# Kernel optimization log

Hardware: AMD Instinct MI355X
Metric: run time of the kernel (lower is better)

The kernel has to match this reference:

```python
import jax, jax.numpy as jnp
import numpy as np

D = 128; H = 8; DH = D // H; L = 3
NA = 8000; NL = 32000; N = NA + NL
E1 = 65536; D_RPE = 5; D_FFN = 2 * D; RF_H = 128


def _ln(x, eps=1e-5):
    mu = x.mean(-1, keepdims=True)
    var = ((x - mu) ** 2).mean(-1, keepdims=True)
    return (x - mu) * jax.lax.rsqrt(var + eps)


def _rms(x, eps=1e-8):
    rms = jnp.sqrt((x ** 2).sum(-1, keepdims=True)) / np.sqrt(x.shape[-1]).astype(np.float32)
    return x / (rms + eps)


def _seg_softmax(logits, idx, n):
    m = jax.ops.segment_max(logits, idx, num_segments=n)
    e = jnp.exp(logits - m[idx])
    s = jax.ops.segment_sum(e, idx, num_segments=n)
    return e / (s[idx] + 1e-16)


def _gat_layer(x, edge_attr, src, dst, mp_W, mp_b, eu_W, eu_b, Wq, Wk, Wv, Wo, fW1, fb1, fW2, fb2):
    E = src.shape[0]
    # build_mem: gather endpoints, project, LN, ReLU
    cat = jnp.concatenate([x[dst], x[src], edge_attr], axis=-1)       # [E, 3D]
    mem = jax.nn.relu(_ln(cat @ mp_W.T + mp_b))                       # [E, D]
    delta = jax.nn.relu(_ln(mem @ eu_W.T + eu_b))                     # edge_update_block
    edge_attr = _ln(edge_attr + delta)                                # edge_norm
    # multi-head edge attention: q from receiver node, k/v from mem
    q = (x[dst] @ Wq.T).reshape(E, H, DH)
    k = (mem @ Wk.T).reshape(E, H, DH)
    v = (mem @ Wv.T).reshape(E, H, DH)
    logits = (q * k).sum(-1) / np.sqrt(DH).astype(np.float32)         # [E, H]
    attn = _seg_softmax(logits, dst, N)                               # segment softmax over receivers
    msg = (attn[..., None] * v).reshape(E, D) @ Wo.T                  # [E, D]
    aggr = jax.ops.segment_sum(msg, dst, num_segments=N)              # scatter-add
    x = _ln(x + aggr)
    h = jax.nn.relu(x @ fW1.T + fb1) @ fW2.T + fb2
    x = _ln(x + h)
    return x, edge_attr


def _ddc(x_cur, prev_list, W1, b1, W2, b2):
    xs = jnp.stack(prev_list, axis=1)                                 # [N, k, D]
    a = jax.nn.gelu(_rms(x_cur) @ W1.T + b1, approximate=False)
    a = jax.nn.softmax(a @ W2.T + b2, axis=-1)                        # [N, k]
    return (a[..., None] * xs).sum(1)


def setup_inputs() -> dict:
    key = jax.random.key(0)
    ks = iter(jax.random.split(key, 48))
    def nrm(shape, fan_in):
        return jax.random.normal(next(ks), shape, jnp.float32) * np.float32(1.0 / np.sqrt(fan_in))
    inp = {}
    inp['actors'] = jax.random.normal(next(ks), (NA, D), jnp.float32)
    inp['lanes'] = jax.random.normal(next(ks), (NL, D), jnp.float32)
    inp['a2a_attr'] = jax.random.normal(next(ks), (E1, D), jnp.float32)
    inp['l2l_attr'] = jax.random.normal(next(ks), (E1, D), jnp.float32)
    inp['a2l_rpe'] = jax.random.normal(next(ks), (E1, D_RPE), jnp.float32)
    inp['rpe_W'] = nrm((D, D_RPE), D_RPE); inp['rpe_b'] = jnp.zeros((D,), jnp.float32)
    inp['mp_W'] = nrm((L, D, 3 * D), 3 * D); inp['mp_b'] = jnp.zeros((L, D), jnp.float32)
    inp['eu_W'] = nrm((L, D, D), D); inp['eu_b'] = jnp.zeros((L, D), jnp.float32)
    inp['Wq'] = nrm((L, D, D), D); inp['Wk'] = nrm((L, D, D), D)
    inp['Wv'] = nrm((L, D, D), D); inp['Wo'] = nrm((L, D, D), D)
    inp['ffn_W1'] = nrm((L, D_FFN, D), D); inp['ffn_b1'] = jnp.zeros((L, D_FFN), jnp.float32)
    inp['ffn_W2'] = nrm((L, D, D_FFN), D_FFN); inp['ffn_b2'] = jnp.zeros((L, D), jnp.float32)
    inp['rf0_W1'] = nrm((RF_H, D), D); inp['rf0_b1'] = jnp.zeros((RF_H,), jnp.float32)
    inp['rf0_W2'] = nrm((1, RF_H), RF_H); inp['rf0_b2'] = jnp.zeros((1,), jnp.float32)
    inp['rf1_W1'] = nrm((RF_H, D), D); inp['rf1_b1'] = jnp.zeros((RF_H,), jnp.float32)
    inp['rf1_W2'] = nrm((2, RF_H), RF_H); inp['rf1_b2'] = jnp.zeros((2,), jnp.float32)
    inp['a2a_edges'] = jax.random.randint(next(ks), (2, E1), 0, N, jnp.int32)
    inp['l2l_edges'] = jax.random.randint(next(ks), (2, E1), 0, N, jnp.int32)
    inp['a2l_edges'] = jax.random.randint(next(ks), (2, E1), 0, N, jnp.int32)
    return inp


def reference(actors, lanes, a2a_attr, l2l_attr, a2l_rpe, rpe_W, rpe_b,
              mp_W, mp_b, eu_W, eu_b, Wq, Wk, Wv, Wo,
              ffn_W1, ffn_b1, ffn_W2, ffn_b2,
              rf0_W1, rf0_b1, rf0_W2, rf0_b2,
              rf1_W1, rf1_b1, rf1_W2, rf1_b2,
              a2a_edges, l2l_edges, a2l_edges):
    token = jnp.concatenate([actors, lanes], axis=0)                  # single scene: actors then lanes
    edge_index = jnp.concatenate([a2a_edges, l2l_edges, a2l_edges], axis=1)
    a2l_attr = jax.nn.relu(_ln(a2l_rpe @ rpe_W.T + rpe_b))            # proj_a2l_l2a_rpe
    edge_attr = jnp.concatenate([a2a_attr, l2l_attr, a2l_attr], axis=0)
    src, dst = edge_index[0], edge_index[1]
    rf = [(rf0_W1, rf0_b1, rf0_W2, rf0_b2), (rf1_W1, rf1_b1, rf1_W2, rf1_b2)]
    token_list = [token]
    for i in range(L):
        token, edge_attr = _gat_layer(token, edge_attr, src, dst,
                                      mp_W[i], mp_b[i], eu_W[i], eu_b[i],
                                      Wq[i], Wk[i], Wv[i], Wo[i],
                                      ffn_W1[i], ffn_b1[i], ffn_W2[i], ffn_b2[i])
        if i < L - 1:
            token = _ddc(token, token_list, *rf[i])
        token_list.append(token)
    return token[:NA], token[NA:]
```

## Files before the change

kernel.cpp:

```cpp
#include <hip/hip_runtime.h>
#include <hip/hip_bf16.h>

using bf16 = __hip_bfloat16;
typedef __bf16 bf16x8 __attribute__((ext_vector_type(8)));
typedef float f32x4 __attribute__((ext_vector_type(4)));

constexpr int DD   = 128;
constexpr int NACT = 8000;
constexpr int NN   = 40000;
constexpr int E1   = 65536;
constexpr int EE   = 3 * E1;

#define BM 128

__device__ __forceinline__ void gload16(const void* g, void* l) {
  __builtin_amdgcn_global_load_lds((const __attribute__((address_space(1))) void*)g,
                                   (__attribute__((address_space(3))) void*)l, 16, 0, 0);
}

__device__ __forceinline__ int edge_dst(int e, const int* e0, const int* e1, const int* e2) {
  int ty = e >> 16, idx = e & 65535;
  const int* ep = (ty == 0) ? e0 : ((ty == 1) ? e1 : e2);
  return ep[E1 + idx];
}
__device__ __forceinline__ int edge_src(int e, const int* e0, const int* e1, const int* e2) {
  int ty = e >> 16, idx = e & 65535;
  const int* ep = (ty == 0) ? e0 : ((ty == 1) ? e1 : e2);
  return ep[idx];
}

__device__ __forceinline__ void mfma_step(const bf16* A0, int lda, const bf16* B0, int ldb,
                                          f32x4 acc[4][4], int wm, int wn, int lane) {
  const int lr = lane & 15;
  const int lk = (lane >> 4) * 8;
  bf16x8 a[4], b[4];
#pragma unroll
  for (int i = 0; i < 4; i++)
    a[i] = *(const bf16x8*)(A0 + (size_t)(wm * 64 + i * 16 + lr) * lda + lk);
#pragma unroll
  for (int j = 0; j < 4; j++)
    b[j] = *(const bf16x8*)(B0 + (size_t)(wn * 64 + j * 16 + lr) * ldb + lk);
#pragma unroll
  for (int i = 0; i < 4; i++)
#pragma unroll
    for (int j = 0; j < 4; j++)
      acc[i][j] = __builtin_amdgcn_mfma_f32_16x16x32_bf16(a[i], b[j], acc[i][j], 0, 0, 0);
}

__device__ __forceinline__ void mfma_swz(const bf16* A0, const bf16* B0,
                                         f32x4 acc[4][4], int wm, int wn, int lane) {
  const int lr = lane & 15;
  const int g  = lane >> 4;
  const int sw = (g ^ ((lr >> 1) & 3)) * 8;
  bf16x8 a[4], b[4];
#pragma unroll
  for (int i = 0; i < 4; i++)
    a[i] = *(const bf16x8*)(A0 + (wm * 64 + i * 16 + lr) * 32 + sw);
#pragma unroll
  for (int j = 0; j < 4; j++)
    b[j] = *(const bf16x8*)(B0 + (wn * 64 + j * 16 + lr) * 32 + sw);
#pragma unroll
  for (int i = 0; i < 4; i++)
#pragma unroll
    for (int j = 0; j < 4; j++)
      acc[i][j] = __builtin_amdgcn_mfma_f32_16x16x32_bf16(a[i], b[j], acc[i][j], 0, 0, 0);
}

__device__ __forceinline__ void mfma_mixed(const bf16* Am, int lda, const bf16* B0,
                                           f32x4 acc[4][4], int wm, int wn, int lane) {
  const int lr = lane & 15;
  const int g  = lane >> 4;
  const int sw = (g ^ ((lr >> 1) & 3)) * 8;
  bf16x8 a[4], b[4];
#pragma unroll
  for (int i = 0; i < 4; i++)
    a[i] = *(const bf16x8*)(Am + (size_t)(wm * 64 + i * 16 + lr) * lda + g * 8);
#pragma unroll
  for (int j = 0; j < 4; j++)
    b[j] = *(const bf16x8*)(B0 + (wn * 64 + j * 16 + lr) * 32 + sw);
#pragma unroll
  for (int i = 0; i < 4; i++)
#pragma unroll
    for (int j = 0; j < 4; j++)
      acc[i][j] = __builtin_amdgcn_mfma_f32_16x16x32_bf16(a[i], b[j], acc[i][j], 0, 0, 0);
}

__device__ __forceinline__ void row_ln_stats(const f32x4 acc[4][4], float* red_s,
                                             float* red_q, int wm, int wn, int lane) {
  const int lr = lane & 15, lg = lane >> 4;
#pragma unroll
  for (int i = 0; i < 4; i++) {
#pragma unroll
    for (int q = 0; q < 4; q++) {
      float s = acc[i][0][q] + acc[i][1][q] + acc[i][2][q] + acc[i][3][q];
      float t = acc[i][0][q] * acc[i][0][q] + acc[i][1][q] * acc[i][1][q]
              + acc[i][2][q] * acc[i][2][q] + acc[i][3][q] * acc[i][3][q];
#pragma unroll
      for (int off = 1; off < 16; off <<= 1) {
        s += __shfl_xor(s, off);
        t += __shfl_xor(t, off);
      }
      if (lr == 0) {
        int row = wm * 64 + i * 16 + lg * 4 + q;
        red_s[wn * 128 + row] = s;
        red_q[wn * 128 + row] = t;
      }
    }
  }
}

template<int LAST>
__global__ __launch_bounds__(256, 3) void k_fused(
    const bf16* __restrict__ Wmp, const bf16* __restrict__ W2,
    const float* __restrict__ mpb, const float* __restrict__ eub,
    bf16* eah, const bf16* __restrict__ x0h,
    const bf16* __restrict__ qh, bf16* vout,
    float* __restrict__ logi, unsigned* __restrict__ nmax,
    const int* __restrict__ e0, const int* __restrict__ e1, const int* __restrict__ e2)
{
  __shared__ __align__(16) char smem[46080];
  bf16* const mem_s = (bf16*)smem;
  bf16* const Bs2   = (bf16*)(smem + 34816);
  float* const red_s = (float*)(smem + 43008);
  float* const red_q = (float*)(smem + 44032);
  int* const sdst = (int*)(smem + 45056);
  int* const ssrc = (int*)(smem + 45568);

  const int tid = threadIdx.x;
  const int bm0 = blockIdx.x * BM;
  const int lane = tid & 63, w = tid >> 6, wm = w >> 1, wn = w & 1;
  const int swzE = ((lane & 3) ^ ((lane >> 3) & 3)) * 8;

  if (tid < 128) sdst[tid] = edge_dst(bm0 + tid, e0, e1, e2);
  else           ssrc[tid - 128] = edge_src(bm0 + tid - 128, e0, e1, e2);
  __syncthreads();
  const int mr0 = w * 16 + (lane >> 2), mr1 = 64 + w * 16 + (lane >> 2);
  const int rd0 = sdst[mr0], rd1 = sdst[mr1];
  const int rs0 = ssrc[mr0], rs1 = ssrc[mr1];
  const bf16* pd0 = x0h + (size_t)rd0 * DD + swzE;
  const bf16* pd1 = x0h + (size_t)rd1 * DD + swzE;
  const bf16* ps0 = x0h + (size_t)rs0 * DD + swzE;
  const bf16* ps1 = x0h + (size_t)rs1 * DD + swzE;
  const bf16* pe0 = eah + (size_t)(bm0 + mr0) * DD + swzE;
  const bf16* pe1 = eah + (size_t)(bm0 + mr1) * DD + swzE;
  const bf16* pB0 = Wmp + (size_t)mr0 * 384 + swzE;
  const bf16* pB1 = Wmp + (size_t)mr1 * 384 + swzE;
  const bf16* pW20 = W2 + (size_t)mr0 * DD + swzE;
  const bf16* pW21 = W2 + (size_t)mr1 * DD + swzE;

  auto STAGE1 = [&](int kb, int buf) {
    const bf16 *a0, *a1;
    const int k4 = (kb & 3) * 32;
    if (kb < 4)      { a0 = pd0 + k4; a1 = pd1 + k4; }
    else if (kb < 8) { a0 = ps0 + k4; a1 = ps1 + k4; }
    else             { a0 = pe0 + k4; a1 = pe1 + k4; }
    char* base = smem + buf * 16384;
    gload16(a0, base + w * 1024);
    gload16(a1, base + 4096 + w * 1024);
    gload16(pB0 + kb * 32, base + 8192 + w * 1024);
    gload16(pB1 + kb * 32, base + 12288 + w * 1024);
  };

  f32x4 acc[4][4] = {};
  STAGE1(0, 0);
  __syncthreads();
  int buf = 0;
#pragma unroll
  for (int kb = 0; kb < 12; kb++) {
    if (kb < 11) STAGE1(kb + 1, buf ^ 1);
    mfma_swz((const bf16*)(smem + buf * 16384), (const bf16*)(smem + buf * 16384 + 8192),
             acc, wm, wn, lane);
    __syncthreads();
    buf ^= 1;
  }

  const int lr = lane & 15, lg = lane >> 4;
  const int colb = wn * 64 + lr;
  const int rowb = wm * 64 + lg * 4;

#pragma unroll
  for (int j = 0; j < 4; j++) {
    float bj = mpb[colb + j * 16];
#pragma unroll
    for (int i = 0; i < 4; i++)
#pragma unroll
      for (int q = 0; q < 4; q++) acc[i][j][q] += bj;
  }
  row_ln_stats(acc, red_s, red_q, wm, wn, lane);
  __syncthreads();
#pragma unroll
  for (int i = 0; i < 4; i++) {
#pragma unroll
    for (int q = 0; q < 4; q++) {
      int row = rowb + i * 16 + q;
      float Sm = red_s[row] + red_s[128 + row];
      float Qs = red_q[row] + red_q[128 + row];
      float mu = Sm * 0.0078125f;
      float var = Qs * 0.0078125f - mu * mu;
      float inv = 1.0f / sqrtf(var + 1e-5f);
#pragma unroll
      for (int j = 0; j < 4; j++)
        mem_s[row * 136 + colb + j * 16] =
            __float2bfloat16(fmaxf((acc[i][j][q] - mu) * inv, 0.f));
    }
  }

  auto GEMM2 = [&](int voff, f32x4 a2[4][4]) {
#pragma unroll 1
    for (int kb = 0; kb < 4; kb++) {
      __syncthreads();
      gload16(pW20 + voff + kb * 32, smem + 34816 + w * 1024);
      gload16(pW21 + voff + kb * 32, smem + 34816 + 4096 + w * 1024);
      __syncthreads();
      mfma_mixed(mem_s + kb * 32, 136, Bs2, a2, wm, wn, lane);
    }
  };
  auto store_tile = [&](bf16* dst) {
#pragma unroll
    for (int c = 0; c < 8; c++) {
      int off = c * 2048 + tid * 8;
      int row = off >> 7, col = off & 127;
      *(uint4*)(dst + (size_t)bm0 * DD + off) = *(uint4*)&mem_s[row * 136 + col];
    }
  };

  if constexpr (LAST == 0) {
    f32x4 acc2[4][4] = {};
    GEMM2(0, acc2);
#pragma unroll
    for (int j = 0; j < 4; j++) {
      float bj = eub[colb + j * 16];
#pragma unroll
      for (int i = 0; i < 4; i++)
#pragma unroll
        for (int q = 0; q < 4; q++) acc2[i][j][q] += bj;
    }
    __syncthreads();
    row_ln_stats(acc2, red_s, red_q, wm, wn, lane);
    __syncthreads();
#pragma unroll
    for (int i = 0; i < 4; i++) {
#pragma unroll
      for (int q = 0; q < 4; q++) {
        int row = rowb + i * 16 + q;
        float Sm = red_s[row] + red_s[128 + row];
        float Qs = red_q[row] + red_q[128 + row];
        float mu = Sm * 0.0078125f;
        float var = Qs * 0.0078125f - mu * mu;
        float inv = 1.0f / sqrtf(var + 1e-5f);
        int r = bm0 + row;
#pragma unroll
        for (int j = 0; j < 4; j++) {
          float d = fmaxf((acc2[i][j][q] - mu) * inv, 0.f);
          float eo = __bfloat162float(eah[(size_t)r * DD + colb + j * 16]);
          acc2[i][j][q] = eo + d;
        }
      }
    }
    __syncthreads();
    row_ln_stats(acc2, red_s, red_q, wm, wn, lane);
    __syncthreads();
#pragma unroll
    for (int i = 0; i < 4; i++) {
#pragma unroll
      for (int q = 0; q < 4; q++) {
        int row = rowb + i * 16 + q;
        float Sm = red_s[row] + red_s[128 + row];
        float Qs = red_q[row] + red_q[128 + row];
        float mu = Sm * 0.0078125f;
        float var = Qs * 0.0078125f - mu * mu;
        float inv = 1.0f / sqrtf(var + 1e-5f);
#pragma unroll
        for (int j = 0; j < 4; j++)
          mem_s[row * 136 + colb + j * 16] =
              __float2bfloat16((acc2[i][j][q] - mu) * inv);
      }
    }
    __syncthreads();
    store_tile(eah);
  } else {
    f32x4 acc2[4][4] = {};
    GEMM2(0, acc2);
#pragma unroll
    for (int i = 0; i < 4; i++) {
#pragma unroll
      for (int q = 0; q < 4; q++) {
        int row = rowb + i * 16 + q;
        int dst = sdst[row];
#pragma unroll
        for (int j = 0; j < 4; j++) {
          int h = wn * 4 + j;
          float qv = __bfloat162float(qh[(size_t)dst * DD + h * 16 + lr]);
          float p = acc2[i][j][q] * qv;
#pragma unroll
          for (int off = 1; off < 16; off <<= 1) p += __shfl_xor(p, off);
          if (lr == 0) {
            p *= 0.25f;
            int e = bm0 + row;
            logi[(size_t)e * 8 + h] = p;
            unsigned u = __float_as_uint(p);
            u = (u & 0x80000000u) ? ~u : (u | 0x80000000u);
            atomicMax(nmax + (size_t)dst * 8 + h, u);
          }
        }
      }
    }
    f32x4 acc3[4][4] = {};
    GEMM2(128 * DD, acc3);
    __syncthreads();
#pragma unroll
    for (int i = 0; i < 4; i++)
#pragma unroll
      for (int q = 0; q < 4; q++) {
        int row = rowb + i * 16 + q;
#pragma unroll
        for (int j = 0; j < 4; j++)
          mem_s[row * 136 + colb + j * 16] = __float2bfloat16(acc3[i][j][q]);
      }
    __syncthreads();
    store_tile(vout);
  }
}

template<int EPI>
__global__ __launch_bounds__(256, 3) void k_gemmG(
    const bf16* __restrict__ A, const bf16* __restrict__ B, void* __restrict__ out,
    const float* __restrict__ bias, const float* __restrict__ aux,
    int M, int K, int lda, int ldc)
{
  __shared__ __align__(16) char smem[36864];
  bf16* const stg = (bf16*)smem;
  float* const red_s = (float*)(smem + 34816);
  float* const red_q = (float*)(smem + 35840);

  const int tid = threadIdx.x, lane = tid & 63, w = tid >> 6;
  const int wm = w >> 1, wn = w & 1;
  const int bm0 = blockIdx.x * BM, bn0 = blockIdx.y * BM;
  const int swzE = ((lane & 3) ^ ((lane >> 3) & 3)) * 8;

  const bf16* pA[2];
  const bf16* pB[2];
#pragma unroll
  for (int r = 0; r < 2; r++) {
    int ra = bm0 + r * 64 + w * 16 + (lane >> 2);
    if (ra > M - 1) ra = M - 1;
    pA[r] = A + (size_t)ra * lda + swzE;
    pB[r] = B + (size_t)(bn0 + r * 64 + w * 16 + (lane >> 2)) * K + swzE;
  }
  auto STAGE = [&](int kb, int buf) {
#pragma unroll
    for (int r = 0; r < 2; r++) {
      gload16(pA[r] + kb * 32, smem + buf * 8192 + r * 4096 + w * 1024);
      gload16(pB[r] + kb * 32, smem + 16384 + buf * 8192 + r * 4096 + w * 1024);
    }
  };

  f32x4 acc[4][4] = {};
  const int KB = K >> 5;
  STAGE(0, 0);
  __syncthreads();
  int buf = 0;
#pragma unroll 1
  for (int kb = 0; kb < KB; kb++) {
    if (kb + 1 < KB) STAGE(kb + 1, buf ^ 1);
    mfma_swz((const bf16*)(smem + buf * 8192), (const bf16*)(smem + 16384 + buf * 8192),
             acc, wm, wn, lane);
    __syncthreads();
    buf ^= 1;
  }

  const int lr = lane & 15, lg = lane >> 4;
  const int colb = wn * 64 + lr;
  const int rowb = wm * 64 + lg * 4;

  if constexpr (EPI == 1 || EPI == 5) {
    if constexpr (EPI == 5) {
#pragma unroll
      for (int j = 0; j < 4; j++) {
        float b = bias[bn0 + colb + j * 16];
#pragma unroll
        for (int i = 0; i < 4; i++)
#pragma unroll
          for (int q = 0; q < 4; q++) acc[i][j][q] = fmaxf(acc[i][j][q] + b, 0.f);
      }
    }
#pragma unroll
    for (int i = 0; i < 4; i++)
#pragma unroll
      for (int q = 0; q < 4; q++) {
        int row = rowb + i * 16 + q;
#pragma unroll
        for (int j = 0; j < 4; j++)
          stg[row * 136 + colb + j * 16] = __float2bfloat16(acc[i][j][q]);
      }
    __syncthreads();
#pragma unroll
    for (int c = 0; c < 8; c++) {
      int off = c * 2048 + tid * 8;
      int row = off >> 7, col = off & 127;
      int r = bm0 + row;
      if (r < M)
        *(uint4*)((bf16*)out + (size_t)r * ldc + bn0 + col) = *(uint4*)&stg[row * 136 + col];
    }
  }

  if constexpr (EPI == 6) {
#pragma unroll
    for (int i = 0; i < 4; i++)
#pragma unroll
      for (int q = 0; q < 4; q++) {
        int r = bm0 + rowb + i * 16 + q;
        if (r < M) {
#pragma unroll
          for (int j = 0; j < 4; j++)
            acc[i][j][q] += bias[colb + j * 16] + aux[(size_t)r * DD + colb + j * 16];
        }
      }
    row_ln_stats(acc, red_s, red_q, wm, wn, lane);
    __syncthreads();
    float* const fstg = (float*)smem;
#pragma unroll
    for (int h = 0; h < 2; h++) {
      if (wm == h) {
#pragma unroll
        for (int i = 0; i < 4; i++)
#pragma unroll
          for (int q = 0; q < 4; q++) {
            int row = rowb + i * 16 + q;
            float Sm = red_s[row] + red_s[128 + row];
            float Qs = red_q[row] + red_q[128 + row];
            float mu = Sm * 0.0078125f;
            float var = Qs * 0.0078125f - mu * mu;
            float inv = 1.0f / sqrtf(var + 1e-5f);
            int rloc = row - h * 64;
#pragma unroll
            for (int j = 0; j < 4; j++)
              fstg[rloc * 132 + colb + j * 16] = (acc[i][j][q] - mu) * inv;
          }
      }
      __syncthreads();
#pragma unroll
      for (int c = 0; c < 8; c++) {
        int boff = c * 4096 + tid * 16;
        int row = boff >> 9, col = (boff & 511) >> 2;
        int r = bm0 + h * 64 + row;
        if (r < M)
          *(float4*)((float*)out + (size_t)r * DD + col) = *(float4*)&fstg[row * 132 + col];
      }
      __syncthreads();
    }
  }
}

__global__ __launch_bounds__(256) void k_msg(
    const bf16* __restrict__ Vh, const bf16* __restrict__ Wo,
    float* __restrict__ aggr, const float* __restrict__ evals, const float* __restrict__ nsum,
    const int* __restrict__ e0, const int* __restrict__ e1, const int* __restrict__ e2)
{
  __shared__ __align__(16) bf16 As[128 * 40];
  __shared__ __align__(16) bf16 Bs[128 * 40];
  __shared__ int sdst[128];
  const int tid = threadIdx.x, lane = tid & 63, w = tid >> 6, wm = w >> 1, wn = w & 1;
  const int bm0 = blockIdx.x * BM;
  if (tid < 128) sdst[tid] = edge_dst(bm0 + tid, e0, e1, e2);
  __syncthreads();
  f32x4 acc[4][4] = {};
#pragma unroll 1
  for (int kb = 0; kb < 4; kb++) {
    const int k0 = kb * 32;
    for (int c = tid; c < 512; c += 256) {
      int row = c >> 2, c8 = (c & 3) * 8;
      int e = bm0 + row;
      int h = (k0 + c8) >> 4;
      uint4 v = *(const uint4*)(Vh + (size_t)e * DD + k0 + c8);
      float at = evals[(size_t)e * 8 + h] / (nsum[(size_t)sdst[row] * 8 + h] + 1e-16f);
      union { uint4 u; bf16 hh[8]; } vv; vv.u = v;
#pragma unroll
      for (int t = 0; t < 8; t++)
        vv.hh[t] = __float2bfloat16(at * __bfloat162float(vv.hh[t]));
      *(uint4*)&As[row * 40 + c8] = vv.u;
      *(uint4*)&Bs[row * 40 + c8] = *(const uint4*)(Wo + (size_t)row * DD + k0 + c8);
    }
    __syncthreads();
    mfma_step(As, 40, Bs, 40, acc, wm, wn, lane);
    __syncthreads();
  }
  const int lr = lane & 15, lg = lane >> 4;
  const int colb = wn * 64 + lr;
  const int rowb = wm * 64 + lg * 4;
#pragma unroll
  for (int i = 0; i < 4; i++)
#pragma unroll
    for (int q = 0; q < 4; q++) {
      int dst = sdst[rowb + i * 16 + q];
#pragma unroll
      for (int j = 0; j < 4; j++)
        atomicAdd(aggr + (size_t)dst * DD + colb + j * 16, acc[i][j][q]);
    }
}

__device__ __forceinline__ float2 ln_pair(float2 v, float eps) {
  float s = v.x + v.y, sq = v.x * v.x + v.y * v.y;
#pragma unroll
  for (int o = 32; o > 0; o >>= 1) {
    s += __shfl_xor(s, o);
    sq += __shfl_xor(sq, o);
  }
  float mu = s * 0.0078125f;
  float var = sq * 0.0078125f - mu * mu;
  float inv = 1.0f / sqrtf(var + eps);
  return make_float2((v.x - mu) * inv, (v.y - mu) * inv);
}

__global__ void k_init_ea(const float* __restrict__ a2a, const float* __restrict__ l2l,
                          const float* __restrict__ rpe, const float* __restrict__ rpeW,
                          const float* __restrict__ rpeb, bf16* __restrict__ eah) {
  int r = blockIdx.x * 4 + (threadIdx.x >> 6);
  int lane = threadIdx.x & 63;
  int ty = r >> 16, idx = r & 65535;
  int c0 = lane * 2;
  float2 y;
  if (ty < 2) {
    y = *(const float2*)((ty == 0 ? a2a : l2l) + (size_t)idx * DD + c0);
  } else {
    float rp0 = rpe[idx * 5 + 0], rp1 = rpe[idx * 5 + 1], rp2 = rpe[idx * 5 + 2];
    float rp3 = rpe[idx * 5 + 3], rp4 = rpe[idx * 5 + 4];
    float2 v;
    v.x = rpeb[c0]     + rp0 * rpeW[c0 * 5]           + rp1 * rpeW[c0 * 5 + 1]
        + rp2 * rpeW[c0 * 5 + 2]     + rp3 * rpeW[c0 * 5 + 3]     + rp4 * rpeW[c0 * 5 + 4];
    v.y = rpeb[c0 + 1] + rp0 * rpeW[(c0 + 1) * 5]     + rp1 * rpeW[(c0 + 1) * 5 + 1]
        + rp2 * rpeW[(c0 + 1) * 5 + 2] + rp3 * rpeW[(c0 + 1) * 5 + 3] + rp4 * rpeW[(c0 + 1) * 5 + 4];
    y = ln_pair(v, 1e-5f);
    y.x = fmaxf(y.x, 0.f);
    y.y = fmaxf(y.y, 0.f);
  }
  size_t o = (size_t)r * DD + c0;
  eah[o] = __float2bfloat16(y.x);
  eah[o + 1] = __float2bfloat16(y.y);
}

__global__ void k_x1(const float* __restrict__ actors, const float* __restrict__ lanesp,
                     const float* __restrict__ aggr, float* __restrict__ x1,
                     bf16* __restrict__ x1h, int R) {
  int r = blockIdx.x * 4 + (threadIdx.x >> 6);
  if (r >= R) return;
  int lane = threadIdx.x & 63;
  int c0 = lane * 2;
  const float* xp = (r < NACT) ? (actors + (size_t)r * DD) : (lanesp + (size_t)(r - NACT) * DD);
  float2 v = *(const float2*)(xp + c0);
  float2 a = *(const float2*)(aggr + (size_t)r * DD + c0);
  v.x += a.x; v.y += a.y;
  float2 y = ln_pair(v, 1e-5f);
  size_t o = (size_t)r * DD + c0;
  *(float2*)(x1 + o) = y;
  x1h[o] = __float2bfloat16(y.x);
  x1h[o + 1] = __float2bfloat16(y.y);
}

__global__ void k_evals(float* __restrict__ logit, const unsigned* __restrict__ nmax,
                        float* __restrict__ nsum,
                        const int* __restrict__ e0, const int* __restrict__ e1,
                        const int* __restrict__ e2) {
  int gid = blockIdx.x * 256 + threadIdx.x;
  int e = gid >> 3, h = gid & 7;
  int dst = edge_dst(e, e0, e1, e2);
  unsigned u = nmax[(size_t)dst * 8 + h];
  float m = (u & 0x80000000u) ? __uint_as_float(u ^ 0x80000000u) : __uint_as_float(~u);
  float v = expf(logit[gid] - m);
  logit[gid] = v;
  atomicAdd(nsum + (size_t)dst * 8 + h, v);
}

__global__ void k_conv(const float* __restrict__ a, bf16* __restrict__ b, int n) {
  int i = blockIdx.x * 256 + threadIdx.x;
  if (i < n) b[i] = __float2bfloat16(a[i]);
}

__global__ void k_x0h(const float* __restrict__ actors, const float* __restrict__ lanesp,
                      bf16* __restrict__ x0h) {
  int gid = blockIdx.x * 256 + threadIdx.x;
  int n = gid >> 7, c = gid & 127;
  float v = (n < NACT) ? actors[(size_t)n * DD + c] : lanesp[(size_t)(n - NACT) * DD + c];
  x0h[gid] = __float2bfloat16(v);
}

extern "C" void kernel_launch(void* const* d_in, const int* in_sizes, int n_in,
                              void* d_out, int out_size, void* d_ws, size_t ws_size,
                              hipStream_t stream) {
  (void)in_sizes; (void)n_in; (void)out_size;
  if (ws_size < (128ull << 20)) return;

  const float* actors = (const float*)d_in[0];
  const float* lanesp = (const float*)d_in[1];
  const float* a2a    = (const float*)d_in[2];
  const float* l2l    = (const float*)d_in[3];
  const float* rpe    = (const float*)d_in[4];
  const float* rpeW   = (const float*)d_in[5];
  const float* rpeb   = (const float*)d_in[6];
  const float* mpW    = (const float*)d_in[7];
  const float* mpb    = (const float*)d_in[8];
  const float* euW    = (const float*)d_in[9];
  const float* eub    = (const float*)d_in[10];
  const float* Wq     = (const float*)d_in[11];
  const float* Wk     = (const float*)d_in[12];
  const float* Wv     = (const float*)d_in[13];
  const float* Wo     = (const float*)d_in[14];
  const float* fW1    = (const float*)d_in[15];
  const float* fb1    = (const float*)d_in[16];
  const float* fW2    = (const float*)d_in[17];
  const float* fb2    = (const float*)d_in[18];
  const int* e0 = (const int*)d_in[27];
  const int* e1 = (const int*)d_in[28];
  const int* e2 = (const int*)d_in[29];

  char* ws = (char*)d_ws;
  bf16* W_MP = (bf16*)ws;
  bf16* W_EU = W_MP + 147456;
  bf16* W_WQ = W_EU + 32768;
  bf16* W_KV = W_WQ + 16384;
  bf16* W_WO = W_KV + 32768;
  bf16* W_F1 = W_WO + 16384;
  bf16* W_F2 = W_F1 + 32768;

  bf16*  X0H = (bf16*)(ws + (1ull << 20));
  bf16*  QH  = (bf16*)(ws + (12ull << 20));
  float* POOL = (float*)(ws + (24ull << 20));
  float*    AGGR = POOL;
  float*    X1   = POOL + 5120000;
  float*    LOGI = POOL + 10240000;
  unsigned* NMAX = (unsigned*)(POOL + 11812864);
  float*    NSUM = POOL + 12132864;
  bf16* EAH = (bf16*)(ws + (80ull << 20));
  bf16* VH  = EAH;
  bf16* X1H = X0H;
  bf16* H1H = EAH;

  k_conv<<<576, 256, 0, stream>>>(mpW, W_MP, 147456);
  k_conv<<<128, 256, 0, stream>>>(euW, W_EU, 32768);
  k_conv<<<64, 256, 0, stream>>>(Wq + 2 * 16384, W_WQ, 16384);
  k_conv<<<64, 256, 0, stream>>>(Wk + 2 * 16384, W_KV, 16384);
  k_conv<<<64, 256, 0, stream>>>(Wv + 2 * 16384, W_KV + 16384, 16384);
  k_conv<<<64, 256, 0, stream>>>(Wo + 2 * 16384, W_WO, 16384);
  k_conv<<<128, 256, 0, stream>>>(fW1 + 2 * 32768, W_F1, 32768);
  k_conv<<<128, 256, 0, stream>>>(fW2 + 2 * 32768, W_F2, 32768);
  k_x0h<<<20000, 256, 0, stream>>>(actors, lanesp, X0H);
  k_init_ea<<<49152, 256, 0, stream>>>(a2a, l2l, rpe, rpeW, rpeb, EAH);

  k_gemmG<1><<<313, 256, 0, stream>>>(X0H, W_WQ, QH, nullptr, nullptr, NN, 128, 128, DD);

  hipMemsetAsync(AGGR, 0, (size_t)NN * DD * 4, stream);
  hipMemsetAsync(NMAX, 0, (size_t)NN * 8 * 4, stream);
  hipMemsetAsync(NSUM, 0, (size_t)NN * 8 * 4, stream);

  for (int i = 0; i < 2; i++) {
    k_fused<0><<<EE / BM, 256, 0, stream>>>(W_MP + i * 49152, W_EU + i * 16384,
        mpb + i * 128, eub + i * 128, EAH, X0H, nullptr, nullptr,
        nullptr, nullptr, e0, e1, e2);
  }
  k_fused<1><<<EE / BM, 256, 0, stream>>>(W_MP + 2 * 49152, W_KV,
      mpb + 2 * 128, nullptr, EAH, X0H, QH, VH, LOGI, NMAX, e0, e1, e2);

  k_evals<<<EE * 8 / 256, 256, 0, stream>>>(LOGI, NMAX, NSUM, e0, e1, e2);

  k_msg<<<EE / BM, 256, 0, stream>>>(VH, W_WO, AGGR, LOGI, NSUM, e0, e1, e2);

  k_x1<<<NN / 4, 256, 0, stream>>>(actors, lanesp, AGGR, X1, X1H, NN);
  k_gemmG<5><<<dim3(313, 2), 256, 0, stream>>>(X1H, W_F1, H1H, fb1 + 2 * 256, nullptr,
                                               NN, 128, 128, 256);
  k_gemmG<6><<<dim3(313, 1), 256, 0, stream>>>(H1H, W_F2, d_out, fb2 + 2 * 128, X1,
                                               NN, 256, 256, DD);
}
```

Baseline: 527.3 us.

## Precompute per-node projections for dst/src parts of edge memory GEMM

The node-dependent parts of the edge projection (x[dst] and x[src] times their weight slices) are now computed once per node in a new k_ps kernel for all three layers. Each edge GEMM then only multiplies the edge attributes (K=128 instead of 384) and adds the gathered per-node partial results before the layer norm. This cuts edge-side MFMA work and the gathered row loads per edge. In exchange it adds a node GEMM, bf16-rounded intermediate tables (a precision change), scattered 2-byte gathers in the epilogue, a larger workspace requirement, and moves the AGGR memset so it can share memory with the tables.

```diff
diff --git a/kernel.cpp b/kernel.cpp
--- a/kernel.cpp
+++ b/kernel.cpp
@@ -109,11 +109,82 @@
   }
 }
 
+__global__ __launch_bounds__(256, 3) void k_ps(
+    const bf16* __restrict__ A, const bf16* __restrict__ Wmp,
+    bf16* __restrict__ ps01, bf16* __restrict__ ps2, int M)
+{
+  __shared__ __align__(16) char smem[36864];
+  bf16* const stg = (bf16*)smem;
+
+  const int tid = threadIdx.x, lane = tid & 63, w = tid >> 6;
+  const int wm = w >> 1, wn = w & 1;
+  const int bm0 = blockIdx.x * BM;
+  const int y = blockIdx.y, l = y >> 1, part = y & 1;
+  const int swzE = ((lane & 3) ^ ((lane >> 3) & 3)) * 8;
+
+  const bf16* pA[2];
+  const bf16* pB[2];
+#pragma unroll
+  for (int r = 0; r < 2; r++) {
+    int ra = bm0 + r * 64 + w * 16 + (lane >> 2);
+    if (ra > M - 1) ra = M - 1;
+    pA[r] = A + (size_t)ra * DD + swzE;
+    int rb = r * 64 + w * 16 + (lane >> 2);
+    pB[r] = Wmp + (size_t)l * 49152 + (size_t)rb * 384 + part * 128 + swzE;
+  }
+  auto STAGE = [&](int kb, int buf) {
+#pragma unroll
+    for (int r = 0; r < 2; r++) {
+      gload16(pA[r] + kb * 32, smem + buf * 8192 + r * 4096 + w * 1024);
+      gload16(pB[r] + kb * 32, smem + 16384 + buf * 8192 + r * 4096 + w * 1024);
+    }
+  };
+
+  f32x4 acc[4][4] = {};
+  STAGE(0, 0);
+  __syncthreads();
+  int buf = 0;
+#pragma unroll 1
+  for (int kb = 0; kb < 4; kb++) {
+    if (kb + 1 < 4) STAGE(kb + 1, buf ^ 1);
+    mfma_swz((const bf16*)(smem + buf * 8192), (const bf16*)(smem + 16384 + buf * 8192),
+             acc, wm, wn, lane);
+    __syncthreads();
+    buf ^= 1;
+  }
+
+  const int lr = lane & 15, lg = lane >> 4;
+  const int colb = wn * 64 + lr;
+  const int rowb = wm * 64 + lg * 4;
+#pragma unroll
+  for (int i = 0; i < 4; i++)
+#pragma unroll
+    for (int q = 0; q < 4; q++) {
+      int row = rowb + i * 16 + q;
+#pragma unroll
+      for (int j = 0; j < 4; j++)
+        stg[row * 136 + colb + j * 16] = __float2bfloat16(acc[i][j][q]);
+    }
+  __syncthreads();
+  bf16* ob;
+  int ldps, coff;
+  if (l < 2) { ob = ps01; ldps = 512; coff = y * 128; }
+  else       { ob = ps2;  ldps = 256; coff = part * 128; }
+#pragma unroll
+  for (int c = 0; c < 8; c++) {
+    int off = c * 2048 + tid * 8;
+    int row = off >> 7, col = off & 127;
+    int r = bm0 + row;
+    if (r < M)
+      *(uint4*)(ob + (size_t)r * ldps + coff + col) = *(uint4*)&stg[row * 136 + col];
+  }
+}
+
 template<int LAST>
 __global__ __launch_bounds__(256, 3) void k_fused(
     const bf16* __restrict__ Wmp, const bf16* __restrict__ W2,
     const float* __restrict__ mpb, const float* __restrict__ eub,
-    bf16* eah, const bf16* __restrict__ x0h,
+    bf16* eah, const bf16* __restrict__ PSd, const bf16* __restrict__ PSs, int ldps,
     const bf16* __restrict__ qh, bf16* vout,
     float* __restrict__ logi, unsigned* __restrict__ nmax,
     const int* __restrict__ e0, const int* __restrict__ e1, const int* __restrict__ e2)
@@ -134,31 +205,20 @@
   if (tid < 128) sdst[tid] = edge_dst(bm0 + tid, e0, e1, e2);
   else           ssrc[tid - 128] = edge_src(bm0 + tid - 128, e0, e1, e2);
   __syncthreads();
-  const int mr0 = w * 16 + (lane >> 2), mr1 = 64 + w * 16 + (lane >> 2);
-  const int rd0 = sdst[mr0], rd1 = sdst[mr1];
-  const int rs0 = ssrc[mr0], rs1 = ssrc[mr1];
-  const bf16* pd0 = x0h + (size_t)rd0 * DD + swzE;
-  const bf16* pd1 = x0h + (size_t)rd1 * DD + swzE;
-  const bf16* ps0 = x0h + (size_t)rs0 * DD + swzE;
-  const bf16* ps1 = x0h + (size_t)rs1 * DD + swzE;
+  const int mr0 = w * 16 + (lane >> 2), mr1 = 64 + mr0;
   const bf16* pe0 = eah + (size_t)(bm0 + mr0) * DD + swzE;
   const bf16* pe1 = eah + (size_t)(bm0 + mr1) * DD + swzE;
-  const bf16* pB0 = Wmp + (size_t)mr0 * 384 + swzE;
-  const bf16* pB1 = Wmp + (size_t)mr1 * 384 + swzE;
+  const bf16* pBc0 = Wmp + (size_t)mr0 * 384 + 256 + swzE;
+  const bf16* pBc1 = Wmp + (size_t)mr1 * 384 + 256 + swzE;
   const bf16* pW20 = W2 + (size_t)mr0 * DD + swzE;
   const bf16* pW21 = W2 + (size_t)mr1 * DD + swzE;
 
   auto STAGE1 = [&](int kb, int buf) {
-    const bf16 *a0, *a1;
-    const int k4 = (kb & 3) * 32;
-    if (kb < 4)      { a0 = pd0 + k4; a1 = pd1 + k4; }
-    else if (kb < 8) { a0 = ps0 + k4; a1 = ps1 + k4; }
-    else             { a0 = pe0 + k4; a1 = pe1 + k4; }
     char* base = smem + buf * 16384;
-    gload16(a0, base + w * 1024);
-    gload16(a1, base + 4096 + w * 1024);
-    gload16(pB0 + kb * 32, base + 8192 + w * 1024);
-    gload16(pB1 + kb * 32, base + 12288 + w * 1024);
+    gload16(pe0 + kb * 32, base + w * 1024);
+    gload16(pe1 + kb * 32, base + 4096 + w * 1024);
+    gload16(pBc0 + kb * 32, base + 8192 + w * 1024);
+    gload16(pBc1 + kb * 32, base + 12288 + w * 1024);
   };
 
   f32x4 acc[4][4] = {};
@@ -166,8 +226,8 @@
   __syncthreads();
   int buf = 0;
 #pragma unroll
-  for (int kb = 0; kb < 12; kb++) {
-    if (kb < 11) STAGE1(kb + 1, buf ^ 1);
+  for (int kb = 0; kb < 4; kb++) {
+    if (kb < 3) STAGE1(kb + 1, buf ^ 1);
     mfma_swz((const bf16*)(smem + buf * 16384), (const bf16*)(smem + buf * 16384 + 8192),
              acc, wm, wn, lane);
     __syncthreads();
@@ -185,6 +245,18 @@
     for (int i = 0; i < 4; i++)
 #pragma unroll
       for (int q = 0; q < 4; q++) acc[i][j][q] += bj;
+  }
+#pragma unroll
+  for (int i = 0; i < 4; i++) {
+#pragma unroll
+    for (int q = 0; q < 4; q++) {
+      int row = rowb + i * 16 + q;
+      const bf16* pd = PSd + (size_t)sdst[row] * ldps + colb;
+      const bf16* ps = PSs + (size_t)ssrc[row] * ldps + colb;
+#pragma unroll
+      for (int j = 0; j < 4; j++)
+        acc[i][j][q] += __bfloat162float(pd[j * 16]) + __bfloat162float(ps[j * 16]);
+    }
   }
   row_ln_stats(acc, red_s, red_q, wm, wn, lane);
   __syncthreads();
@@ -588,7 +660,7 @@
                               void* d_out, int out_size, void* d_ws, size_t ws_size,
                               hipStream_t stream) {
   (void)in_sizes; (void)n_in; (void)out_size;
-  if (ws_size < (128ull << 20)) return;
+  if (ws_size < (150ull << 20)) return;
 
   const float* actors = (const float*)d_in[0];
   const float* lanesp = (const float*)d_in[1];
@@ -627,11 +699,13 @@
   float* POOL = (float*)(ws + (24ull << 20));
   float*    AGGR = POOL;
   float*    X1   = POOL + 5120000;
+  bf16*     PS01 = (bf16*)POOL;
   float*    LOGI = POOL + 10240000;
   unsigned* NMAX = (unsigned*)(POOL + 11812864);
   float*    NSUM = POOL + 12132864;
   bf16* EAH = (bf16*)(ws + (80ull << 20));
   bf16* VH  = EAH;
+  bf16* PS2 = (bf16*)(ws + (128ull << 20));
   bf16* X1H = X0H;
   bf16* H1H = EAH;
 
@@ -648,17 +722,22 @@
 
   k_gemmG<1><<<313, 256, 0, stream>>>(X0H, W_WQ, QH, nullptr, nullptr, NN, 128, 128, DD);
 
-  hipMemsetAsync(AGGR, 0, (size_t)NN * DD * 4, stream);
+  k_ps<<<dim3(313, 6), 256, 0, stream>>>(X0H, W_MP, PS01, PS2, NN);
+
   hipMemsetAsync(NMAX, 0, (size_t)NN * 8 * 4, stream);
   hipMemsetAsync(NSUM, 0, (size_t)NN * 8 * 4, stream);
 
   for (int i = 0; i < 2; i++) {
     k_fused<0><<<EE / BM, 256, 0, stream>>>(W_MP + i * 49152, W_EU + i * 16384,
-        mpb + i * 128, eub + i * 128, EAH, X0H, nullptr, nullptr,
-        nullptr, nullptr, e0, e1, e2);
+        mpb + i * 128, eub + i * 128, EAH,
+        PS01 + i * 256, PS01 + i * 256 + 128, 512,
+        nullptr, nullptr, nullptr, nullptr, e0, e1, e2);
   }
   k_fused<1><<<EE / BM, 256, 0, stream>>>(W_MP + 2 * 49152, W_KV,
-      mpb + 2 * 128, nullptr, EAH, X0H, QH, VH, LOGI, NMAX, e0, e1, e2);
+      mpb + 2 * 128, nullptr, EAH, PS2, PS2 + 128, 256,
+      QH, VH, LOGI, NMAX, e0, e1, e2);
+
+  hipMemsetAsync(AGGR, 0, (size_t)NN * DD * 4, stream);
 
   k_evals<<<EE * 8 / 256, 256, 0, stream>>>(LOGI, NMAX, NSUM, e0, e1, e2);
 
```

Result: slower. 647.0 us (+22.7%).
